# Optimization experiments

Hardware: AMD Instinct MI355X
Metric: run time of the kernel (lower is better)

## Reference

```python
import jax, jax.numpy as jnp
import numpy as np

B, T, D, V, L, HM = 4, 2048, 128, 64, 12, 512
EPS = 1e-5
SCALE = float(np.sqrt(D))


def setup_inputs() -> dict:
    key = jax.random.key(0)
    ks = jax.random.split(key, 12)
    s = 0.02
    x = jax.random.randint(ks[0], (B, T), 0, V)
    pos_emb = jax.random.normal(ks[1], (T, D), jnp.float32) * s
    # per-layer params stacked on leading L axis; Linear weights in torch (out,in) layout
    Wq = jax.random.normal(ks[2], (L, D, D), jnp.float32) * s
    Wk = jax.random.normal(ks[3], (L, D, D), jnp.float32) * s
    Wv = jax.random.normal(ks[4], (L, D, D), jnp.float32) * s
    ln1_g = jnp.ones((L, D), jnp.float32)
    ln1_b = jnp.zeros((L, D), jnp.float32)
    W1 = jax.random.normal(ks[5], (L, HM, D), jnp.float32) * s
    b1 = jnp.zeros((L, HM), jnp.float32)
    W2 = jax.random.normal(ks[6], (L, D, HM), jnp.float32) * s
    b2 = jnp.zeros((L, D), jnp.float32)
    ln2_g = jnp.ones((L, D), jnp.float32)
    ln2_b = jnp.zeros((L, D), jnp.float32)
    Wro = jax.random.normal(ks[7], (1, D), jnp.float32) * s
    bro = jnp.zeros((1,), jnp.float32)
    return dict(x=x, pos_emb=pos_emb, Wq=Wq, Wk=Wk, Wv=Wv, ln1_g=ln1_g, ln1_b=ln1_b,
                W1=W1, b1=b1, W2=W2, b2=b2, ln2_g=ln2_g, ln2_b=ln2_b, Wro=Wro, bro=bro)


def _layernorm(h, g, b):
    mu = jnp.mean(h, axis=-1, keepdims=True)
    var = jnp.mean(jnp.square(h - mu), axis=-1, keepdims=True)
    return (h - mu) * jax.lax.rsqrt(var + EPS) * g + b


def _token_embeddings(x):
    # -(c - x)^2 / 2 over class ids, zero-padded up to D
    ar = jnp.arange(V, dtype=jnp.float32)  # [V]
    leave = -jnp.square(ar - x[..., None].astype(jnp.float32)) * 0.5  # [B,T,V]
    return jnp.pad(leave, ((0, 0), (0, 0), (0, D - V)))  # [B,T,D]


def _forward(x, pos_emb, Wq, Wk, Wv, ln1_g, ln1_b, W1, b1, W2, b2, ln2_g, ln2_b, Wro, bro):
    H = _token_embeddings(x) + pos_emb[None]  # [B,T,D]

    def step(Hc, p):
        wq, wk, wv, g1, be1, w1, bb1, w2, bb2, g2, be2 = p
        H1 = _layernorm(Hc, g1, be1)
        q = H1 @ wq.T
        k = H1 @ wk.T
        v = H1 @ wv.T
        scores = jnp.einsum('bid,bjd->bij', q, k) / SCALE  # [B,T,T]
        attn = jax.nn.softmax(scores, axis=-1)
        Hc = Hc + jnp.einsum('bij,bjd->bid', attn, v)
        H2 = _layernorm(Hc, g2, be2)
        Hc = Hc + (jax.nn.gelu(H2 @ w1.T + bb1, approximate=False) @ w2.T + bb2)
        return Hc, None

    H, _ = jax.lax.scan(step, H, (Wq, Wk, Wv, ln1_g, ln1_b, W1, b1, W2, b2, ln2_g, ln2_b))
    pred = H @ Wro.T + bro  # [B,T,1]
    return pred[:, :, 0]


def reference(x, pos_emb, Wq, Wk, Wv, ln1_g, ln1_b, W1, b1, W2, b2, ln2_g, ln2_b, Wro, bro):
    return _forward(x, pos_emb, Wq, Wk, Wv, ln1_g, ln1_b, W1, b1, W2, b2, ln2_g, ln2_b, Wro, bro)
```

## Files before the change

### kernel.cpp

```cpp
#include <hip/hip_runtime.h>
#include <math.h>

#define D 128
#define T 2048
#define BATCH 4
#define HMID 512
#define NLAYER 12

#define KSPLIT 8
#define KPB (T / KSPLIT)

#if defined(__has_builtin)
#if __has_builtin(__builtin_amdgcn_global_load_lds)
#define USE_GLL 1
#endif
#endif
#ifndef USE_GLL
#define USE_GLL 0
#endif

typedef unsigned short u16;
typedef __attribute__((ext_vector_type(8))) short bf16x8;
typedef __attribute__((ext_vector_type(16))) float f32x16;

__device__ inline u16 f2bf(float x) {
    unsigned u = __builtin_bit_cast(unsigned, x);
    return (u16)((u + 0x7FFFu + ((u >> 16) & 1u)) >> 16);
}
__device__ inline float bf2f(u16 v) {
    return __builtin_bit_cast(float, (unsigned)v << 16);
}
__device__ inline unsigned pkt(float a, float b) {
    return (__builtin_bit_cast(unsigned, a) >> 16) |
           (__builtin_bit_cast(unsigned, b) & 0xFFFF0000u);
}

__device__ inline void ln_stats32(const float (*Ct)[132], float* mu_s, float* rs_s, int tid) {
    const int q = tid >> 3, e8 = tid & 7;
    float s = 0.f;
#pragma unroll
    for (int c = 0; c < 16; c++) s += Ct[q][e8 * 16 + c];
    s += __shfl_xor(s, 1); s += __shfl_xor(s, 2); s += __shfl_xor(s, 4);
    float mu = s * (1.f / D);
    float s2 = 0.f;
#pragma unroll
    for (int c = 0; c < 16; c++) {
        float d0 = Ct[q][e8 * 16 + c] - mu;
        s2 += d0 * d0;
    }
    s2 += __shfl_xor(s2, 1); s2 += __shfl_xor(s2, 2); s2 += __shfl_xor(s2, 4);
    if (e8 == 0) { mu_s[q] = mu; rs_s[q] = rsqrtf(s2 * (1.f / D) + 1e-5f); }
}

__device__ inline void build_as(const float (*Ct)[132], const float* mu_s, const float* rs_s,
                                const float* __restrict__ g, const float* __restrict__ bb,
                                u16* As, int tid) {
    const int row = tid >> 3, e8 = tid & 7;
    const float mu = mu_s[row], rs = rs_s[row];
#pragma unroll
    for (int cc = 0; cc < 2; cc++) {
        int c = e8 * 2 + cc;
        u16 tmp[8];
#pragma unroll
        for (int j = 0; j < 8; j++) {
            int d = c * 8 + j;
            tmp[j] = f2bf((Ct[row][d] - mu) * rs * g[d] + bb[d]);
        }
        *(uint4*)&As[((size_t)c * 32 + (row ^ (c & 7))) * 8] = *(uint4*)tmp;
    }
}

__device__ inline void stage_w(const u16* __restrict__ W, int ldw, u16* Wst, int tid) {
#pragma unroll
    for (int i = 0; i < 8; i++) {
        int ci = tid + 256 * i;
        int row = ci >> 4, c = ci & 15;
        *(uint4*)&Wst[((size_t)c * 128 + (row ^ c)) * 8] =
            *(const uint4*)(W + (size_t)row * ldw + c * 8);
    }
}

__device__ inline f32x16 mm_32x128(const u16* As, const u16* Wst, int wv, int ql, int h) {
    f32x16 a;
#pragma unroll
    for (int r = 0; r < 16; r++) a[r] = 0.f;
#pragma unroll
    for (int s = 0; s < 8; s++) {
        int ch = 2 * s + h;
        bf16x8 af = *(const bf16x8*)&As[((size_t)ch * 32 + (ql ^ (ch & 7))) * 8];
        bf16x8 bf = *(const bf16x8*)&Wst[((size_t)ch * 128 + ((wv * 32 + ql) ^ ch)) * 8];
        a = __builtin_amdgcn_mfma_f32_32x32x16_bf16(af, bf, a, 0, 0, 0);
    }
    return a;
}

__device__ inline void qkv_phase(const u16* As, const u16* __restrict__ Wqkvl, u16* Wst,
                                 u16* __restrict__ qb, u16* __restrict__ kb,
                                 u16* __restrict__ vt, int m0, int tid) {
    const int wv = tid >> 6, l = tid & 63, h = l >> 5, ql = l & 31;
    const int bbk = m0 >> 11;
    const int tl0 = m0 & (T - 1);
#pragma unroll
    for (int sl = 0; sl < 3; sl++) {
        __syncthreads();
        stage_w(Wqkvl + (size_t)sl * 128 * D, D, Wst, tid);
        __syncthreads();
        f32x16 a = mm_32x128(As, Wst, wv, ql, h);
        const int n = wv * 32 + ql;
        if (sl == 2) {
            u16* dst = vt + (size_t)bbk * D * T + (size_t)n * T + tl0;
#pragma unroll
            for (int g = 0; g < 4; g++) {
                ushort4 o;
                o.x = f2bf(a[4 * g + 0]);
                o.y = f2bf(a[4 * g + 1]);
                o.z = f2bf(a[4 * g + 2]);
                o.w = f2bf(a[4 * g + 3]);
                *(ushort4*)(dst + 8 * g + 4 * h) = o;
            }
        } else {
            u16* dst = (sl == 0) ? qb : kb;
#pragma unroll
            for (int r = 0; r < 16; r++) {
                int row = (r & 3) + 8 * (r >> 2) + 4 * h;
                dst[(size_t)(m0 + row) * D + n] = f2bf(a[r]);
            }
        }
    }
}

__global__ __launch_bounds__(256) void conv_all(const float* __restrict__ Wq,
                                                const float* __restrict__ Wk,
                                                const float* __restrict__ Wv,
                                                const float* __restrict__ W1,
                                                const float* __restrict__ W2,
                                                u16* __restrict__ Wqkv,
                                                u16* __restrict__ W1b,
                                                u16* __restrict__ W2b, float qscale) {
    const int NQ = NLAYER * 3 * D * D;
    const int NW = NLAYER * HMID * D;
    int idx = blockIdx.x * 256 + threadIdx.x;
    if (idx < NQ) {
        int lN = idx / (3 * D * D);
        int rem = idx - lN * (3 * D * D);
        int s = rem >> 14;
        int off = rem & 16383;
        const float* src = (s == 0) ? Wq : ((s == 1) ? Wk : Wv);
        Wqkv[idx] = f2bf(src[lN * 16384 + off] * ((s == 0) ? qscale : 1.f));
    } else if (idx < NQ + NW) {
        W1b[idx - NQ] = f2bf(W1[idx - NQ]);
    } else if (idx < NQ + 2 * NW) {
        W2b[idx - NQ - NW] = f2bf(W2[idx - NQ - NW]);
    }
}

__global__ __launch_bounds__(256, 2) void embed_qkv(const int* __restrict__ x,
                                                    const float* __restrict__ pos,
                                                    const float* __restrict__ g1,
                                                    const float* __restrict__ b1g,
                                                    const u16* __restrict__ Wqkv0,
                                                    u16* __restrict__ qb, u16* __restrict__ kb,
                                                    u16* __restrict__ vt,
                                                    float* __restrict__ H) {
    __shared__ float Ct[32][132];
    __shared__ float mu_s[32], rs_s[32];
    __shared__ u16 As[16 * 32 * 8];
    __shared__ u16 Wst[16 * 128 * 8];
    const int tid = threadIdx.x;
    const int m0 = blockIdx.x * 32;
    {
        const int d = tid & 127, rr = tid >> 7;
#pragma unroll
        for (int i = 0; i < 16; i++) {
            int row = rr * 16 + i;
            int tok = m0 + row;
            int t = tok & (T - 1);
            float e = 0.f;
            if (d < 64) {
                float diff = (float)d - (float)x[tok];
                e = -0.5f * diff * diff;
            }
            float v = e + pos[(size_t)t * D + d];
            Ct[row][d] = v;
            H[(size_t)tok * D + d] = v;
        }
    }
    __syncthreads();
    ln_stats32(Ct, mu_s, rs_s, tid);
    __syncthreads();
    build_as(Ct, mu_s, rs_s, g1, b1g, As, tid);
    qkv_phase(As, Wqkv0, Wst, qb, kb, vt, m0, tid);
}

__global__ __launch_bounds__(256, 2) void attn_mfma(const u16* __restrict__ qg,
                                                    const u16* __restrict__ kg,
                                                    const u16* __restrict__ vtg,
                                                    u16* __restrict__ Op,
                                                    float* __restrict__ ml) {
    __shared__ u16 Ks[128 * 128];
    __shared__ u16 Vt[128 * 128];
    const int tid = threadIdx.x;
    const int w = tid >> 6;
    const int l = tid & 63;
    const int h = l >> 5;
    const int ql = l & 31;
    const int qblk = blockIdx.x;
    const int ks = blockIdx.y;
    const int b = qblk >> 4;

    const size_t qrow = (size_t)qblk * 128 + w * 32 + ql;
    bf16x8 qf[8];
#pragma unroll
    for (int c = 0; c < 8; c++)
        qf[c] = *(const bf16x8*)(qg + qrow * D + c * 16 + h * 8);

    f32x16 ot[4];
#pragma unroll
    for (int t = 0; t < 4; t++)
#pragma unroll
        for (int r = 0; r < 16; r++) ot[t][r] = 0.f;
    float l_run = 0.f;

    const u16* kgb = kg + (size_t)b * T * D;
    const u16* vtb = vtg + (size_t)b * D * T;
    const int qsw = ql & 7;

    for (int kt = 0; kt < KPB / 128; kt++) {
        const int kbase = ks * KPB + kt * 128;
        __syncthreads();
#if USE_GLL
#pragma unroll
        for (int i = 0; i < 8; i++) {
            int s = i * 256 + w * 64 + l;
            int row = s >> 4, ch = (s & 15) ^ (row & 7);
            __builtin_amdgcn_global_load_lds(
                (const __attribute__((address_space(1))) void*)(kgb + (size_t)(kbase + row) * D + ch * 8),
                (__attribute__((address_space(3))) void*)&Ks[(i * 256 + w * 64) * 8], 16, 0, 0);
        }
#pragma unroll
        for (int i = 0; i < 8; i++) {
            int s = i * 256 + w * 64 + l;
            int dd = s >> 4, ch = (s & 15) ^ (dd & 7);
            __builtin_amdgcn_global_load_lds(
                (const __attribute__((address_space(1))) void*)(vtb + (size_t)dd * T + kbase + ch * 8),
                (__attribute__((address_space(3))) void*)&Vt[(i * 256 + w * 64) * 8], 16, 0, 0);
        }
#else
#pragma unroll
        for (int i = 0; i < 8; i++) {
            int s = tid + i * 256;
            int row = s >> 4, ch = (s & 15) ^ (row & 7);
            *(uint4*)&Ks[(size_t)s * 8] = *(const uint4*)(kgb + (size_t)(kbase + row) * D + ch * 8);
            *(uint4*)&Vt[(size_t)s * 8] = *(const uint4*)(vtb + (size_t)row * T + kbase + ch * 8);
        }
#endif
        __syncthreads();
        uint2 pk[4][4];
        float rs = 0.f;
#pragma unroll
        for (int s4 = 0; s4 < 4; s4++) {
            const int krow = s4 * 32 + ql;
            f32x16 st;
#pragma unroll
            for (int r = 0; r < 16; r++) st[r] = 0.f;
#pragma unroll
            for (int c = 0; c < 8; c++) {
                bf16x8 kf = *(const bf16x8*)&Ks[((size_t)krow * 16 + ((2 * c + h) ^ qsw)) * 8];
                st = __builtin_amdgcn_mfma_f32_32x32x16_bf16(kf, qf[c], st, 0, 0, 0);
            }
#pragma unroll
            for (int r = 0; r < 16; r++) {
                float p = exp2f(st[r]);
                st[r] = p;
                rs += p;
            }
#pragma unroll
            for (int g = 0; g < 4; g++) {
                pk[s4][g].x = pkt(st[4 * g + 0], st[4 * g + 1]);
                pk[s4][g].y = pkt(st[4 * g + 2], st[4 * g + 3]);
            }
        }
        rs += __shfl_xor(rs, 32);
        l_run += rs;
#pragma unroll
        for (int c = 0; c < 8; c++) {
            const int s4 = c >> 1, cc = c & 1;
            uint2 own = h ? pk[s4][2 * cc + 1] : pk[s4][2 * cc];
            uint2 snd = h ? pk[s4][2 * cc] : pk[s4][2 * cc + 1];
            uint2 rcv;
            rcv.x = (unsigned)__shfl_xor((int)snd.x, 32);
            rcv.y = (unsigned)__shfl_xor((int)snd.y, 32);
            uint4 fr;
            fr.x = h ? rcv.x : own.x;
            fr.y = h ? rcv.y : own.y;
            fr.z = h ? own.x : rcv.x;
            fr.w = h ? own.y : rcv.y;
            bf16x8 pf = __builtin_bit_cast(bf16x8, fr);
            const int kch = 2 * c + h;
#pragma unroll
            for (int t = 0; t < 4; t++) {
                bf16x8 vf = *(const bf16x8*)&Vt[((size_t)(t * 32 + ql) * 16 + (kch ^ qsw)) * 8];
                ot[t] = __builtin_amdgcn_mfma_f32_32x32x16_bf16(vf, pf, ot[t], 0, 0, 0);
            }
        }
    }
    size_t base = (((size_t)(qblk * KSPLIT + ks)) * 4 + w) * (128 * 32);
#pragma unroll
    for (int t = 0; t < 4; t++)
#pragma unroll
        for (int r = 0; r < 16; r++) {
            int dd = (r & 3) + 8 * (r >> 2) + 4 * h + 32 * t;
            Op[base + (size_t)dd * 32 + ql] = f2bf(ot[t][r]);
        }
    if (h == 0) {
        int qi = w * 32 + ql;
        ml[(size_t)(qblk * KSPLIT + ks) * 256 + 128 + qi] = l_run;
    }
}

template <int LAST>
__global__ __launch_bounds__(256, 2) void layer_tail(
    const u16* __restrict__ Op, const float* __restrict__ ml,
    float* __restrict__ H,
    const float* __restrict__ g2, const float* __restrict__ b2l,
    const u16* __restrict__ W1l, const float* __restrict__ b1l,
    const u16* __restrict__ W2l, const float* __restrict__ b2bias,
    const float* __restrict__ g1n, const float* __restrict__ b1n,
    const u16* __restrict__ Wqkvn,
    u16* __restrict__ qb, u16* __restrict__ kb, u16* __restrict__ vt,
    const float* __restrict__ Wro, const float* __restrict__ bro,
    float* __restrict__ outp) {
    __shared__ float Ct[32][132];
    __shared__ float mu_s[32], rs_s[32];
    __shared__ u16 As[16 * 32 * 8];
    __shared__ u16 midS[16 * 32 * 8];
    __shared__ u16 Wst[16 * 128 * 8];

    const int tid = threadIdx.x;
    const int bid = blockIdx.x;
    const int qblk = bid >> 2;
    const int wq = bid & 3;
    const int m0 = bid * 32;
    const int wv = tid >> 6;
    const int l = tid & 63;
    const int h = l >> 5;
    const int ql = l & 31;

    {
        const int dg = tid >> 5;
        float L = 0.f;
#pragma unroll
        for (int ks = 0; ks < KSPLIT; ks++)
            L += ml[(size_t)(qblk * KSPLIT + ks) * 256 + 128 + wq * 32 + ql];
        float invL = 1.f / L;
        float acc[16];
#pragma unroll
        for (int i = 0; i < 16; i++) acc[i] = 0.f;
#pragma unroll
        for (int ks = 0; ks < KSPLIT; ks++) {
            size_t base = (((size_t)(qblk * KSPLIT + ks)) * 4 + wq) * (128 * 32);
#pragma unroll
            for (int i = 0; i < 16; i++)
                acc[i] += bf2f(Op[base + (size_t)(dg * 16 + i) * 32 + ql]);
        }
#pragma unroll
        for (int i = 0; i < 16; i++) Ct[ql][dg * 16 + i] = acc[i] * invL;
    }
    __syncthreads();
    {
        const int d = tid & 127, rr = tid >> 7;
#pragma unroll
        for (int i = 0; i < 16; i++) {
            int row = rr * 16 + i;
            Ct[row][d] += H[(size_t)(m0 + row) * D + d];
        }
    }
    __syncthreads();
    ln_stats32(Ct, mu_s, rs_s, tid);
    __syncthreads();
    build_as(Ct, mu_s, rs_s, g2, b2l, As, tid);
    f32x16 a2;
#pragma unroll
    for (int r = 0; r < 16; r++) a2[r] = 0.f;
    for (int kc = 0; kc < 4; kc++) {
        __syncthreads();
        stage_w(W1l + (size_t)kc * 128 * D, D, Wst, tid);
        __syncthreads();
        f32x16 a = mm_32x128(As, Wst, wv, ql, h);
        const int nl = wv * 32 + ql;
        const int ch2 = nl >> 3, sub = nl & 7;
        const float bv = b1l[kc * 128 + nl];
#pragma unroll
        for (int r = 0; r < 16; r++) {
            int row = (r & 3) + 8 * (r >> 2) + 4 * h;
            float v = a[r] + bv;
            v = 0.5f * v * (1.f + erff(v * 0.7071067811865475f));
            midS[((size_t)ch2 * 32 + (row ^ (ch2 & 7))) * 8 + sub] = f2bf(v);
        }
        __syncthreads();
        stage_w(W2l + (size_t)kc * 128, HMID, Wst, tid);
        __syncthreads();
#pragma unroll
        for (int s = 0; s < 8; s++) {
            int ch = 2 * s + h;
            bf16x8 af = *(const bf16x8*)&midS[((size_t)ch * 32 + (ql ^ (ch & 7))) * 8];
            bf16x8 bf = *(const bf16x8*)&Wst[((size_t)ch * 128 + ((wv * 32 + ql) ^ ch)) * 8];
            a2 = __builtin_amdgcn_mfma_f32_32x32x16_bf16(af, bf, a2, 0, 0, 0);
        }
    }
    __syncthreads();
    {
        const int col = wv * 32 + ql;
        const float bv = b2bias[col];
#pragma unroll
        for (int r = 0; r < 16; r++) {
            int row = (r & 3) + 8 * (r >> 2) + 4 * h;
            float v = a2[r] + bv + Ct[row][col];
            Ct[row][col] = v;
            H[(size_t)(m0 + row) * D + col] = v;
        }
    }
    __syncthreads();
    if (LAST) {
        const int q = tid >> 3, e8 = tid & 7;
        float s = 0.f;
#pragma unroll
        for (int c = 0; c < 16; c++) s += Ct[q][e8 * 16 + c] * Wro[e8 * 16 + c];
        s += __shfl_xor(s, 1); s += __shfl_xor(s, 2); s += __shfl_xor(s, 4);
        if (e8 == 0) outp[m0 + q] = s + bro[0];
    } else {
        ln_stats32(Ct, mu_s, rs_s, tid);
        __syncthreads();
        build_as(Ct, mu_s, rs_s, g1n, b1n, As, tid);
        qkv_phase(As, Wqkvn, Wst, qb, kb, vt, m0, tid);
    }
}

extern "C" void kernel_launch(void* const* d_in, const int* in_sizes, int n_in,
                              void* d_out, int out_size, void* d_ws, size_t ws_size,
                              hipStream_t stream) {
    const int* x = (const int*)d_in[0];
    const float* pos = (const float*)d_in[1];
    const float* Wq = (const float*)d_in[2];
    const float* Wk = (const float*)d_in[3];
    const float* Wv = (const float*)d_in[4];
    const float* ln1g = (const float*)d_in[5];
    const float* ln1b = (const float*)d_in[6];
    const float* W1 = (const float*)d_in[7];
    const float* b1 = (const float*)d_in[8];
    const float* W2 = (const float*)d_in[9];
    const float* b2 = (const float*)d_in[10];
    const float* ln2g = (const float*)d_in[11];
    const float* ln2b = (const float*)d_in[12];
    const float* Wro = (const float*)d_in[13];
    const float* bro = (const float*)d_in[14];
    float* out = (float*)d_out;

    const size_t NTOK = (size_t)BATCH * T;
    const size_t HSZ = NTOK * D;
    float* ws = (float*)d_ws;
    float* H = ws;
    u16* qb = (u16*)(ws + HSZ);
    u16* kb = (u16*)(ws + HSZ + HSZ / 2);
    u16* vt = (u16*)(ws + 2 * HSZ);
    u16* Op = (u16*)(ws + 2 * HSZ + HSZ / 2);
    float* mlbuf = ws + 7 * HSZ;
    u16* Wqkv = (u16*)(ws + 7 * HSZ + 131072);
    u16* W1b = Wqkv + (size_t)NLAYER * 3 * D * D;
    u16* W2b = W1b + (size_t)NLAYER * HMID * D;

    const float qscale = 1.4426950408889634f / 11.313708498984761f;

    conv_all<<<dim3(8448), 256, 0, stream>>>(Wq, Wk, Wv, W1, W2, Wqkv, W1b, W2b, qscale);
    embed_qkv<<<dim3(256), 256, 0, stream>>>(x, pos, ln1g, ln1b, Wqkv, qb, kb, vt, H);

    for (int lay = 0; lay < NLAYER; lay++) {
        attn_mfma<<<dim3(64, KSPLIT), 256, 0, stream>>>(qb, kb, vt, Op, mlbuf);
        if (lay < NLAYER - 1) {
            layer_tail<0><<<dim3(256), 256, 0, stream>>>(
                Op, mlbuf, H,
                ln2g + (size_t)lay * D, ln2b + (size_t)lay * D,
                W1b + (size_t)lay * HMID * D, b1 + (size_t)lay * HMID,
                W2b + (size_t)lay * D * HMID, b2 + (size_t)lay * D,
                ln1g + (size_t)(lay + 1) * D, ln1b + (size_t)(lay + 1) * D,
                Wqkv + (size_t)(lay + 1) * 3 * D * D,
                qb, kb, vt, Wro, bro, nullptr);
        } else {
            layer_tail<1><<<dim3(256), 256, 0, stream>>>(
                Op, mlbuf, H,
                ln2g + (size_t)lay * D, ln2b + (size_t)lay * D,
                W1b + (size_t)lay * HMID * D, b1 + (size_t)lay * HMID,
                W2b + (size_t)lay * D * HMID, b2 + (size_t)lay * D,
                ln1g, ln1b, Wqkv,
                qb, kb, vt, Wro, bro, out);
        }
    }
}
```

Baseline: 593.5 us.

## Double-buffer weight staging with async global-to-LDS loads in layer tail

Replaces synchronous weight staging with global_load_lds async copies into a row-major swizzled layout. The layer tail kernel now double-buffers W1, W2 and next-layer QKV weights so the loads overlap the MFMA work. It also fuses LayerNorm stats into the A-tile build, vectorises the split-K partial reduction, and swaps exact erf GELU for a tanh approximation. The two weight buffers enlarge LDS use and cut occupancy to one block per CU. The GELU change also alters numerics slightly, and sync correctness of the async loads relies on __syncthreads covering the LDS DMA.

```diff
diff --git a/kernel.cpp b/kernel.cpp
--- a/kernel.cpp
+++ b/kernel.cpp
@@ -34,29 +34,30 @@
     return (__builtin_bit_cast(unsigned, a) >> 16) |
            (__builtin_bit_cast(unsigned, b) & 0xFFFF0000u);
 }
-
-__device__ inline void ln_stats32(const float (*Ct)[132], float* mu_s, float* rs_s, int tid) {
-    const int q = tid >> 3, e8 = tid & 7;
+__device__ inline float gelu_f(float v) {
+    float y = 0.7978845608028654f * v * fmaf(0.044715f, v * v, 1.f);
+    float e = exp2f(2.885390081777927f * y);
+    return v * (1.f - 1.f / (e + 1.f));
+}
+
+__device__ inline void build_as_fused(const float (*Ct)[132],
+                                      const float* __restrict__ g,
+                                      const float* __restrict__ bb,
+                                      u16* As, int tid) {
+    const int row = tid >> 3, e8 = tid & 7;
     float s = 0.f;
 #pragma unroll
-    for (int c = 0; c < 16; c++) s += Ct[q][e8 * 16 + c];
+    for (int c = 0; c < 16; c++) s += Ct[row][e8 * 16 + c];
     s += __shfl_xor(s, 1); s += __shfl_xor(s, 2); s += __shfl_xor(s, 4);
     float mu = s * (1.f / D);
     float s2 = 0.f;
 #pragma unroll
     for (int c = 0; c < 16; c++) {
-        float d0 = Ct[q][e8 * 16 + c] - mu;
+        float d0 = Ct[row][e8 * 16 + c] - mu;
         s2 += d0 * d0;
     }
     s2 += __shfl_xor(s2, 1); s2 += __shfl_xor(s2, 2); s2 += __shfl_xor(s2, 4);
-    if (e8 == 0) { mu_s[q] = mu; rs_s[q] = rsqrtf(s2 * (1.f / D) + 1e-5f); }
-}
-
-__device__ inline void build_as(const float (*Ct)[132], const float* mu_s, const float* rs_s,
-                                const float* __restrict__ g, const float* __restrict__ bb,
-                                u16* As, int tid) {
-    const int row = tid >> 3, e8 = tid & 7;
-    const float mu = mu_s[row], rs = rs_s[row];
+    float rs = rsqrtf(s2 * (1.f / D) + 1e-5f);
 #pragma unroll
     for (int cc = 0; cc < 2; cc++) {
         int c = e8 * 2 + cc;
@@ -70,17 +71,29 @@
     }
 }
 
-__device__ inline void stage_w(const u16* __restrict__ W, int ldw, u16* Wst, int tid) {
+__device__ inline void stage_w_async(const u16* __restrict__ W, int ldw, u16* Wst, int tid) {
+    const int w = tid >> 6, l = tid & 63;
+#if USE_GLL
 #pragma unroll
     for (int i = 0; i < 8; i++) {
-        int ci = tid + 256 * i;
-        int row = ci >> 4, c = ci & 15;
-        *(uint4*)&Wst[((size_t)c * 128 + (row ^ c)) * 8] =
-            *(const uint4*)(W + (size_t)row * ldw + c * 8);
-    }
+        int s = i * 256 + w * 64 + l;
+        int row = s >> 4, ch = (s & 15) ^ (row & 7);
+        __builtin_amdgcn_global_load_lds(
+            (const __attribute__((address_space(1))) void*)(W + (size_t)row * ldw + ch * 8),
+            (__attribute__((address_space(3))) void*)&Wst[(i * 256 + w * 64) * 8], 16, 0, 0);
+    }
+#else
+#pragma unroll
+    for (int i = 0; i < 8; i++) {
+        int s = tid + i * 256;
+        int row = s >> 4, ch = (s & 15) ^ (row & 7);
+        *(uint4*)&Wst[(size_t)s * 8] = *(const uint4*)(W + (size_t)row * ldw + ch * 8);
+    }
+#endif
 }
 
 __device__ inline f32x16 mm_32x128(const u16* As, const u16* Wst, int wv, int ql, int h) {
+    const int n = wv * 32 + ql, nsw = n & 7;
     f32x16 a;
 #pragma unroll
     for (int r = 0; r < 16; r++) a[r] = 0.f;
@@ -88,45 +101,10 @@
     for (int s = 0; s < 8; s++) {
         int ch = 2 * s + h;
         bf16x8 af = *(const bf16x8*)&As[((size_t)ch * 32 + (ql ^ (ch & 7))) * 8];
-        bf16x8 bf = *(const bf16x8*)&Wst[((size_t)ch * 128 + ((wv * 32 + ql) ^ ch)) * 8];
+        bf16x8 bf = *(const bf16x8*)&Wst[((size_t)n * 16 + (ch ^ nsw)) * 8];
         a = __builtin_amdgcn_mfma_f32_32x32x16_bf16(af, bf, a, 0, 0, 0);
     }
     return a;
-}
-
-__device__ inline void qkv_phase(const u16* As, const u16* __restrict__ Wqkvl, u16* Wst,
-                                 u16* __restrict__ qb, u16* __restrict__ kb,
-                                 u16* __restrict__ vt, int m0, int tid) {
-    const int wv = tid >> 6, l = tid & 63, h = l >> 5, ql = l & 31;
-    const int bbk = m0 >> 11;
-    const int tl0 = m0 & (T - 1);
-#pragma unroll
-    for (int sl = 0; sl < 3; sl++) {
-        __syncthreads();
-        stage_w(Wqkvl + (size_t)sl * 128 * D, D, Wst, tid);
-        __syncthreads();
-        f32x16 a = mm_32x128(As, Wst, wv, ql, h);
-        const int n = wv * 32 + ql;
-        if (sl == 2) {
-            u16* dst = vt + (size_t)bbk * D * T + (size_t)n * T + tl0;
-#pragma unroll
-            for (int g = 0; g < 4; g++) {
-                ushort4 o;
-                o.x = f2bf(a[4 * g + 0]);
-                o.y = f2bf(a[4 * g + 1]);
-                o.z = f2bf(a[4 * g + 2]);
-                o.w = f2bf(a[4 * g + 3]);
-                *(ushort4*)(dst + 8 * g + 4 * h) = o;
-            }
-        } else {
-            u16* dst = (sl == 0) ? qb : kb;
-#pragma unroll
-            for (int r = 0; r < 16; r++) {
-                int row = (r & 3) + 8 * (r >> 2) + 4 * h;
-                dst[(size_t)(m0 + row) * D + n] = f2bf(a[r]);
-            }
-        }
-    }
 }
 
 __global__ __launch_bounds__(256) void conv_all(const float* __restrict__ Wq,
@@ -163,11 +141,11 @@
                                                     u16* __restrict__ vt,
                                                     float* __restrict__ H) {
     __shared__ float Ct[32][132];
-    __shared__ float mu_s[32], rs_s[32];
     __shared__ u16 As[16 * 32 * 8];
     __shared__ u16 Wst[16 * 128 * 8];
     const int tid = threadIdx.x;
     const int m0 = blockIdx.x * 32;
+    const int wv = tid >> 6, l = tid & 63, h = l >> 5, ql = l & 31;
     {
         const int d = tid & 127, rr = tid >> 7;
 #pragma unroll
@@ -186,10 +164,32 @@
         }
     }
     __syncthreads();
-    ln_stats32(Ct, mu_s, rs_s, tid);
-    __syncthreads();
-    build_as(Ct, mu_s, rs_s, g1, b1g, As, tid);
-    qkv_phase(As, Wqkv0, Wst, qb, kb, vt, m0, tid);
+    build_as_fused(Ct, g1, b1g, As, tid);
+#pragma unroll
+    for (int sl = 0; sl < 3; sl++) {
+        __syncthreads();
+        stage_w_async(Wqkv0 + (size_t)sl * 128 * D, D, Wst, tid);
+        __syncthreads();
+        f32x16 a = mm_32x128(As, Wst, wv, ql, h);
+        const int n = wv * 32 + ql;
+        if (sl == 2) {
+            u16* dst = vt + (size_t)(m0 >> 11) * D * T + (size_t)n * T + (m0 & (T - 1));
+#pragma unroll
+            for (int g = 0; g < 4; g++) {
+                ushort4 o;
+                o.x = f2bf(a[4 * g + 0]); o.y = f2bf(a[4 * g + 1]);
+                o.z = f2bf(a[4 * g + 2]); o.w = f2bf(a[4 * g + 3]);
+                *(ushort4*)(dst + 8 * g + 4 * h) = o;
+            }
+        } else {
+            u16* dst = (sl == 0) ? qb : kb;
+#pragma unroll
+            for (int r = 0; r < 16; r++) {
+                int row = (r & 3) + 8 * (r >> 2) + 4 * h;
+                dst[(size_t)(m0 + row) * D + n] = f2bf(a[r]);
+            }
+        }
+    }
 }
 
 __global__ __launch_bounds__(256, 2) void attn_mfma(const u16* __restrict__ qg,
@@ -319,7 +319,7 @@
 }
 
 template <int LAST>
-__global__ __launch_bounds__(256, 2) void layer_tail(
+__global__ __launch_bounds__(256, 1) void layer_tail(
     const u16* __restrict__ Op, const float* __restrict__ ml,
     float* __restrict__ H,
     const float* __restrict__ g2, const float* __restrict__ b2l,
@@ -331,10 +331,10 @@
     const float* __restrict__ Wro, const float* __restrict__ bro,
     float* __restrict__ outp) {
     __shared__ float Ct[32][132];
-    __shared__ float mu_s[32], rs_s[32];
+    __shared__ float Linv[32];
     __shared__ u16 As[16 * 32 * 8];
     __shared__ u16 midS[16 * 32 * 8];
-    __shared__ u16 Wst[16 * 128 * 8];
+    __shared__ u16 WstBuf[2][16 * 128 * 8];
 
     const int tid = threadIdx.x;
     const int bid = blockIdx.x;
@@ -345,26 +345,41 @@
     const int l = tid & 63;
     const int h = l >> 5;
     const int ql = l & 31;
-
+    u16* Wst0 = &WstBuf[0][0];
+    u16* Wst1 = &WstBuf[1][0];
+
+    stage_w_async(W1l, D, Wst0, tid);
+    stage_w_async(W2l, HMID, Wst1, tid);
+
+    if (tid < 32) {
+        float L = 0.f;
+#pragma unroll
+        for (int ks = 0; ks < KSPLIT; ks++)
+            L += ml[(size_t)(qblk * KSPLIT + ks) * 256 + 128 + wq * 32 + tid];
+        Linv[tid] = 1.f / L;
+    }
+    __syncthreads();
     {
-        const int dg = tid >> 5;
-        float L = 0.f;
-#pragma unroll
-        for (int ks = 0; ks < KSPLIT; ks++)
-            L += ml[(size_t)(qblk * KSPLIT + ks) * 256 + 128 + wq * 32 + ql];
-        float invL = 1.f / L;
+        const int dd = tid >> 1, qh = tid & 1;
         float acc[16];
 #pragma unroll
         for (int i = 0; i < 16; i++) acc[i] = 0.f;
 #pragma unroll
         for (int ks = 0; ks < KSPLIT; ks++) {
-            size_t base = (((size_t)(qblk * KSPLIT + ks)) * 4 + wq) * (128 * 32);
-#pragma unroll
-            for (int i = 0; i < 16; i++)
-                acc[i] += bf2f(Op[base + (size_t)(dg * 16 + i) * 32 + ql]);
-        }
-#pragma unroll
-        for (int i = 0; i < 16; i++) Ct[ql][dg * 16 + i] = acc[i] * invL;
+            const u16* p = Op + (((size_t)(qblk * KSPLIT + ks)) * 4 + wq) * (128 * 32) +
+                           (size_t)dd * 32 + qh * 16;
+            uint4 v0 = *(const uint4*)p;
+            uint4 v1 = *(const uint4*)(p + 8);
+            const u16* u0 = (const u16*)&v0;
+            const u16* u1 = (const u16*)&v1;
+#pragma unroll
+            for (int j = 0; j < 8; j++) {
+                acc[j] += bf2f(u0[j]);
+                acc[8 + j] += bf2f(u1[j]);
+            }
+        }
+#pragma unroll
+        for (int i = 0; i < 16; i++) Ct[qh * 16 + i][dd] = acc[i] * Linv[qh * 16 + i];
     }
     __syncthreads();
     {
@@ -376,39 +391,41 @@
         }
     }
     __syncthreads();
-    ln_stats32(Ct, mu_s, rs_s, tid);
+    build_as_fused(Ct, g2, b2l, As, tid);
     __syncthreads();
-    build_as(Ct, mu_s, rs_s, g2, b2l, As, tid);
+
     f32x16 a2;
 #pragma unroll
     for (int r = 0; r < 16; r++) a2[r] = 0.f;
+#pragma unroll
     for (int kc = 0; kc < 4; kc++) {
-        __syncthreads();
-        stage_w(W1l + (size_t)kc * 128 * D, D, Wst, tid);
-        __syncthreads();
-        f32x16 a = mm_32x128(As, Wst, wv, ql, h);
-        const int nl = wv * 32 + ql;
-        const int ch2 = nl >> 3, sub = nl & 7;
-        const float bv = b1l[kc * 128 + nl];
-#pragma unroll
-        for (int r = 0; r < 16; r++) {
-            int row = (r & 3) + 8 * (r >> 2) + 4 * h;
-            float v = a[r] + bv;
-            v = 0.5f * v * (1.f + erff(v * 0.7071067811865475f));
-            midS[((size_t)ch2 * 32 + (row ^ (ch2 & 7))) * 8 + sub] = f2bf(v);
-        }
-        __syncthreads();
-        stage_w(W2l + (size_t)kc * 128, HMID, Wst, tid);
-        __syncthreads();
-#pragma unroll
-        for (int s = 0; s < 8; s++) {
-            int ch = 2 * s + h;
-            bf16x8 af = *(const bf16x8*)&midS[((size_t)ch * 32 + (ql ^ (ch & 7))) * 8];
-            bf16x8 bf = *(const bf16x8*)&Wst[((size_t)ch * 128 + ((wv * 32 + ql) ^ ch)) * 8];
-            a2 = __builtin_amdgcn_mfma_f32_32x32x16_bf16(af, bf, a2, 0, 0, 0);
-        }
-    }
-    __syncthreads();
+        if (kc >= 1) stage_w_async(W2l + (size_t)kc * 128, HMID, Wst1, tid);
+        {
+            f32x16 a = mm_32x128(As, Wst0, wv, ql, h);
+            const int nl = wv * 32 + ql;
+            const int ch2 = nl >> 3, sub = nl & 7;
+            const float bv = b1l[kc * 128 + nl];
+#pragma unroll
+            for (int r = 0; r < 16; r++) {
+                int row = (r & 3) + 8 * (r >> 2) + 4 * h;
+                midS[((size_t)ch2 * 32 + (row ^ (ch2 & 7))) * 8 + sub] = f2bf(gelu_f(a[r] + bv));
+            }
+        }
+        __syncthreads();
+        if (kc < 3) stage_w_async(W1l + (size_t)(kc + 1) * 128 * D, D, Wst0, tid);
+        else if (!LAST) stage_w_async(Wqkvn, D, Wst0, tid);
+        {
+            const int n = wv * 32 + ql, nsw = n & 7;
+#pragma unroll
+            for (int s = 0; s < 8; s++) {
+                int ch = 2 * s + h;
+                bf16x8 af = *(const bf16x8*)&midS[((size_t)ch * 32 + (ql ^ (ch & 7))) * 8];
+                bf16x8 bf = *(const bf16x8*)&WstBuf[1][((size_t)n * 16 + (ch ^ nsw)) * 8];
+                a2 = __builtin_amdgcn_mfma_f32_32x32x16_bf16(af, bf, a2, 0, 0, 0);
+            }
+        }
+        __syncthreads();
+    }
     {
         const int col = wv * 32 + ql;
         const float bv = b2bias[col];
@@ -429,10 +446,42 @@
         s += __shfl_xor(s, 1); s += __shfl_xor(s, 2); s += __shfl_xor(s, 4);
         if (e8 == 0) outp[m0 + q] = s + bro[0];
     } else {
-        ln_stats32(Ct, mu_s, rs_s, tid);
-        __syncthreads();
-        build_as(Ct, mu_s, rs_s, g1n, b1n, As, tid);
-        qkv_phase(As, Wqkvn, Wst, qb, kb, vt, m0, tid);
+        build_as_fused(Ct, g1n, b1n, As, tid);
+        __syncthreads();
+        stage_w_async(Wqkvn + (size_t)128 * D, D, Wst1, tid);
+        {
+            f32x16 a = mm_32x128(As, Wst0, wv, ql, h);
+            const int n = wv * 32 + ql;
+#pragma unroll
+            for (int r = 0; r < 16; r++) {
+                int row = (r & 3) + 8 * (r >> 2) + 4 * h;
+                qb[(size_t)(m0 + row) * D + n] = f2bf(a[r]);
+            }
+        }
+        __syncthreads();
+        stage_w_async(Wqkvn + (size_t)256 * D, D, Wst0, tid);
+        {
+            f32x16 a = mm_32x128(As, Wst1, wv, ql, h);
+            const int n = wv * 32 + ql;
+#pragma unroll
+            for (int r = 0; r < 16; r++) {
+                int row = (r & 3) + 8 * (r >> 2) + 4 * h;
+                kb[(size_t)(m0 + row) * D + n] = f2bf(a[r]);
+            }
+        }
+        __syncthreads();
+        {
+            f32x16 a = mm_32x128(As, Wst0, wv, ql, h);
+            const int n = wv * 32 + ql;
+            u16* dst = vt + (size_t)(m0 >> 11) * D * T + (size_t)n * T + (m0 & (T - 1));
+#pragma unroll
+            for (int g = 0; g < 4; g++) {
+                ushort4 o;
+                o.x = f2bf(a[4 * g + 0]); o.y = f2bf(a[4 * g + 1]);
+                o.z = f2bf(a[4 * g + 2]); o.w = f2bf(a[4 * g + 3]);
+                *(ushort4*)(dst + 8 * g + 4 * h) = o;
+            }
+        }
     }
 }
 
```

Result: faster. 563.6 us (-5.0%).
